# Optimization experiments

Measured on AMD Instinct MI355X. Metric: run time of the kernel, lower is better.

## Reference

```python
import jax, jax.numpy as jnp
import numpy as np

H = 16          # num_heads
HD = 64         # head_dim = latent_dim // num_heads
RHD = 32        # rope_head_dim = head_dim // 2
NHD = 32        # nope_head_dim
Q_LAT = 256     # latent_dim // compression_ratio
KV_LAT = 204    # xf_latent_dim // (compression_ratio + 1)
MAX_LEN = 2048
THETA = 10000.0
EPS = 1e-5


def _rope_tables():
    half = RHD // 2  # 16
    freqs = 1.0 / THETA ** (np.arange(half, dtype=np.float32) / half)
    t = np.arange(MAX_LEN, dtype=np.float32)
    ang = np.outer(t, freqs)  # (MAX_LEN, half)
    return jnp.asarray(np.cos(ang)), jnp.asarray(np.sin(ang))

COS, SIN = _rope_tables()


def _ln(x, g, b):
    m = jnp.mean(x, axis=-1, keepdims=True)
    v = jnp.var(x, axis=-1, keepdims=True)
    return (x - m) * jax.lax.rsqrt(v + EPS) * g + b


def _rope(t, cos, sin):
    # t: (..., L, RHD); cos/sin: (L, RHD//2); interleaved even/odd convention
    ev, od = t[..., 0::2], t[..., 1::2]
    oe = ev * cos - od * sin
    oo = ev * sin + od * cos
    return jnp.stack([oe, oo], axis=-1).reshape(t.shape)


def setup_inputs() -> dict:
    key = jax.random.key(0)
    ks = jax.random.split(key, 12)
    D = 1024
    s = 0.02
    return {
        "x": jax.random.normal(ks[0], (2, 2048, D), jnp.float32),
        "xf": jax.random.normal(ks[1], (2, 2048, D), jnp.float32),
        "Wqc": jax.random.normal(ks[2], (D, Q_LAT), jnp.float32) * s,
        "gq": jnp.ones((Q_LAT,), jnp.float32),
        "bq": jnp.zeros((Q_LAT,), jnp.float32),
        "Wq_rope": jax.random.normal(ks[3], (Q_LAT, H * RHD), jnp.float32) * s,
        "Wq_nope": jax.random.normal(ks[4], (Q_LAT, H * NHD), jnp.float32) * s,
        "Wkvc": jax.random.normal(ks[5], (D, KV_LAT), jnp.float32) * s,
        "gkv": jnp.ones((KV_LAT,), jnp.float32),
        "bkv": jnp.zeros((KV_LAT,), jnp.float32),
        "Wk_nope": jax.random.normal(ks[6], (KV_LAT, H * NHD), jnp.float32) * s,
        "Wv": jax.random.normal(ks[7], (KV_LAT, H * HD), jnp.float32) * s,
        "Wkr": jax.random.normal(ks[8], (D, RHD), jnp.float32) * s,
        "Wo": jax.random.normal(ks[9], (D, D), jnp.float32) * s,
        "bo": jnp.zeros((D,), jnp.float32),
    }


def reference(x, xf, Wqc, gq, bq, Wq_rope, Wq_nope, Wkvc, gkv, bkv, Wk_nope, Wv, Wkr, Wo, bo):
    B, T, D = x.shape
    S = xf.shape[1]

    # query path: compress -> LN -> decoupled decompress
    ql = _ln(x @ Wqc, gq, bq)                                   # (B,T,Q_LAT)
    q_nope = (ql @ Wq_nope).reshape(B, T, H, NHD).transpose(0, 2, 1, 3)  # (B,H,T,NHD)
    q_rope = (ql @ Wq_rope).reshape(B, T, H, RHD).transpose(0, 2, 1, 3)  # (B,H,T,RHD)

    # key/value path: compress -> LN -> decompress; shared single rope head
    kvl = _ln(xf @ Wkvc, gkv, bkv)                              # (B,S,KV_LAT)
    k_nope = (kvl @ Wk_nope).reshape(B, S, H, NHD).transpose(0, 2, 1, 3)  # (B,H,S,NHD)
    v = (kvl @ Wv).reshape(B, S, H, HD).transpose(0, 2, 1, 3)   # (B,H,S,HD)
    k_rope = (xf @ Wkr).reshape(B, S, 1, RHD).transpose(0, 2, 1, 3)       # (B,1,S,RHD)

    q_rope = _rope(q_rope, COS[:T], SIN[:T])
    k_rope = _rope(k_rope, COS[:S], SIN[:S]) / H
    k_rope = jnp.broadcast_to(k_rope, (B, H, S, RHD))

    q = jnp.concatenate([q_nope, q_rope], axis=-1)              # (B,H,T,HD)
    k = jnp.concatenate([k_nope, k_rope], axis=-1)              # (B,H,S,HD)

    scale = 1.0 / jnp.sqrt(jnp.asarray(HD, q.dtype))
    scores = jnp.einsum("bhtd,bhsd->bhts", q, k) * scale
    attn = jax.nn.softmax(scores, axis=-1)
    o = jnp.einsum("bhts,bhsd->bhtd", attn, v)                  # (B,H,T,HD)
    o = o.transpose(0, 2, 1, 3).reshape(B, T, H * HD)
    return o @ Wo + bo
```

## Files before the change

### kernel.cpp

```cpp
#include <hip/hip_runtime.h>
#include <hip/hip_bf16.h>
#include <math.h>

#define SEQ 2048

typedef __bf16 bf16x8 __attribute__((ext_vector_type(8)));
typedef float  f32x4  __attribute__((ext_vector_type(4)));

#if __has_builtin(__builtin_amdgcn_exp2f)
#define EXP2(x) __builtin_amdgcn_exp2f(x)
#else
#define EXP2(x) exp2f(x)
#endif

__device__ __forceinline__ unsigned short f2bf(float f) {
  __bf16 h = (__bf16)f;
  return __builtin_bit_cast(unsigned short, h);
}

__device__ __forceinline__ void gload16(const unsigned short* g, unsigned short* l) {
  __builtin_amdgcn_global_load_lds(
      (const __attribute__((address_space(1))) void*)g,
      (__attribute__((address_space(3))) void*)l, 16, 0, 0);
}

__device__ __forceinline__ unsigned cvtpk(float lo, float hi) {
  unsigned r;
  asm("v_cvt_pk_bf16_f32 %0, %1, %2" : "=v"(r) : "v"(lo), "v"(hi));
  return r;
}
__device__ __forceinline__ void plswap32(unsigned &a, unsigned &b) {
  asm("v_permlane32_swap_b32 %0, %1" : "+v"(a), "+v"(b));
}
__device__ __forceinline__ void plswap16(unsigned &a, unsigned &b) {
  asm("v_permlane16_swap_b32 %0, %1" : "+v"(a), "+v"(b));
}

#define CLOG (0.125f * 1.44269504f)

struct WPrep {
  const float* src[8];
  unsigned short* dst[8];
  int K[8], N[8], NR[8], KC[8], nb[8];
  float2* cst;
};

__global__ __launch_bounds__(256) void wprep_kernel(WPrep p)
{
  __shared__ float tile[32][33];
  int bid = blockIdx.x;
  if (bid < 128) {
    const int idx = bid * 256 + threadIdx.x;
    const int pos = idx >> 4, i = idx & 15;
    const float freq = EXP2(-(float)i * 0.8304820237f);
    const float ang = (float)pos * freq;
    p.cst[idx] = make_float2(cosf(ang), sinf(ang));
    return;
  }
  bid -= 128;
  int di = 0;
  while (bid >= p.nb[di]) { bid -= p.nb[di]; ++di; }
  const float* src = p.src[di];
  unsigned short* dst = p.dst[di];
  const int K = p.K[di], N = p.N[di], KC = p.KC[di];
  const int nkx = KC >> 5;
  const int k0 = (bid % nkx) * 32, n0 = (bid / nkx) * 32;
  const int tx = threadIdx.x & 31, ty = threadIdx.x >> 5;
  for (int r = ty; r < 32; r += 8) {
    const int k = k0 + r, n = n0 + tx;
    tile[r][tx] = (k < K && n < N) ? src[(long)k * N + n] : 0.0f;
  }
  __syncthreads();
  for (int r = ty; r < 32; r += 8) {
    const int n = n0 + r, k = k0 + tx;
    dst[(long)n * KC + k] = f2bf(tile[tx][r]);
  }
}

template <int EPI, bool AF32>
__device__ __forceinline__ void gemm_body(
    unsigned short* smem,
    const void* __restrict__ Av, const unsigned short* __restrict__ BT,
    const float* __restrict__ bias, const float2* __restrict__ cst,
    void* __restrict__ C0v, void* __restrict__ C1v, int K, int N,
    int bx, int by)
{
  unsigned short* As = smem;
  unsigned short* Bs = smem + 2 * 128 * 32;
  const int tid = threadIdx.x;
  const int w = tid >> 6, lane = tid & 63;
  const int ln16 = lane & 15, quad = lane >> 4;
  const int wm = (w >> 1) * 64, wn = (w & 1) * 64;
  const int m0 = by * 128, n0 = bx * 128;
  const int rr = tid >> 2, cc = (tid & 3) * 8;

  const unsigned short* A = (const unsigned short*)Av;

  auto stageB = [&](int ib, int k0) {
    gload16(&BT[(long)(n0 + rr)      * K + k0 + cc], &Bs[ib * 4096 + rr * 32 + cc]);
    gload16(&BT[(long)(n0 + 64 + rr) * K + k0 + cc], &Bs[ib * 4096 + (64 + rr) * 32 + cc]);
  };
  auto stageAbf = [&](int ib, int k0) {
    gload16(&A[(long)(m0 + rr)      * K + k0 + cc], &As[ib * 4096 + rr * 32 + cc]);
    gload16(&A[(long)(m0 + 64 + rr) * K + k0 + cc], &As[ib * 4096 + (64 + rr) * 32 + cc]);
  };

  f32x4 acc[4][4];
#pragma unroll
  for (int i = 0; i < 4; ++i)
#pragma unroll
    for (int j = 0; j < 4; ++j)
#pragma unroll
      for (int r = 0; r < 4; ++r) acc[i][j][r] = 0.0f;

  stageB(0, 0);
  stageAbf(0, 0);

  int ib = 0;
  for (int k0 = 0; k0 < K; k0 += 32, ib ^= 1) {
    __syncthreads();
    const int kn = k0 + 32;
    if (kn < K) { stageB(ib ^ 1, kn); stageAbf(ib ^ 1, kn); }
    bf16x8 fa[4], fb[4];
#pragma unroll
    for (int i = 0; i < 4; ++i) fa[i] = *(const bf16x8*)&As[ib * 4096 + (wm + i * 16 + ln16) * 32 + quad * 8];
#pragma unroll
    for (int j = 0; j < 4; ++j) fb[j] = *(const bf16x8*)&Bs[ib * 4096 + (wn + j * 16 + ln16) * 32 + quad * 8];
#pragma unroll
    for (int i = 0; i < 4; ++i)
#pragma unroll
      for (int j = 0; j < 4; ++j)
        acc[i][j] = __builtin_amdgcn_mfma_f32_16x16x32_bf16(fa[i], fb[j], acc[i][j], 0, 0, 0);
  }

  if (EPI == 5 && n0 >= 512) {
    __syncthreads();
#pragma unroll
    for (int i = 0; i < 4; ++i) {
      const int rl = wm + i * 16 + quad * 4;
#pragma unroll
      for (int j = 0; j < 4; ++j) {
        const int cl = wn + j * 16 + ln16;
        ushort4 u;
        u.x = f2bf(acc[i][j][0]); u.y = f2bf(acc[i][j][1]);
        u.z = f2bf(acc[i][j][2]); u.w = f2bf(acc[i][j][3]);
        *(ushort4*)&smem[cl * 132 + rl] = u;
      }
    }
    __syncthreads();
    unsigned short* vT = (unsigned short*)C1v;
    const int b = m0 >> 11, sbase = m0 & (SEQ - 1);
    for (int q = tid; q < 128 * 16; q += 256) {
      const int cl = q >> 4, sch = (q & 15) * 8;
      bf16x8 val = *(const bf16x8*)&smem[cl * 132 + sch];
      const int c = (n0 - 512) + cl;
      const int hh = c >> 6, dd = c & 63;
      *(bf16x8*)&vT[((long)(b * 16 + hh) * 64 + dd) * SEQ + sbase + sch] = val;
    }
    return;
  }
#pragma unroll
  for (int i = 0; i < 4; ++i) {
    const int row0 = m0 + wm + i * 16 + quad * 4;
#pragma unroll
    for (int j = 0; j < 4; ++j) {
      const int col = n0 + wn + j * 16 + ln16;
      if (EPI == 3) {
        if (n0 < 512) {
          unsigned short* qn = (unsigned short*)C0v;
#pragma unroll
          for (int r = 0; r < 4; ++r) qn[(long)(row0 + r) * 512 + col] = f2bf(acc[i][j][r] * CLOG);
        } else {
          unsigned short* qr = (unsigned short*)C1v;
          const int c = col - 512;
          const int d = c & 31;
#pragma unroll
          for (int r = 0; r < 4; ++r) {
            const float v = acc[i][j][r];
            const float p = __shfl_xor(v, 1);
            const float2 t = cst[((row0 + r) & (SEQ - 1)) * 16 + (d >> 1)];
            const float o = ((d & 1) == 0) ? (v * t.x - p * t.y) : (p * t.y + v * t.x);
            qr[(long)(row0 + r) * 512 + c] = f2bf(o * CLOG);
          }
        }
      } else if (EPI == 5) {
        unsigned short* kn = (unsigned short*)C0v;
#pragma unroll
        for (int r = 0; r < 4; ++r) kn[(long)(row0 + r) * 512 + col] = f2bf(acc[i][j][r]);
      }
    }
  }
}

template <int E0, bool AF0, int E1, bool AF1>
__global__ __launch_bounds__(256) void gemm_dual(
    const void* __restrict__ A0, const unsigned short* __restrict__ BT0,
    void* __restrict__ C00, void* __restrict__ C01, int K0, int N0, int nx0,
    const void* __restrict__ A1, const unsigned short* __restrict__ BT1,
    void* __restrict__ C10, void* __restrict__ C11, int K1, int N1,
    const float2* __restrict__ cst)
{
  __shared__ unsigned short smem[16896];
  if (blockIdx.z == 0) {
    if ((int)blockIdx.x >= nx0) return;
    gemm_body<E0, AF0>(smem, A0, BT0, nullptr, cst, C00, C01, K0, N0, blockIdx.x, blockIdx.y);
  } else {
    gemm_body<E1, AF1>(smem, A1, BT1, nullptr, cst, C10, C11, K1, N1, blockIdx.x, blockIdx.y);
  }
}

template <int EPI, bool AF32>
__device__ __forceinline__ void gemm_body64(
    unsigned short* smem,
    const void* __restrict__ Av, const unsigned short* __restrict__ BT,
    const float* __restrict__ bias, const float2* __restrict__ cst,
    void* __restrict__ C0v, void* __restrict__ C1v, int K, int N,
    int bx, int by)
{
  unsigned short* As = smem;
  unsigned short* Bs = smem + 2 * 64 * 32;
  const int tid = threadIdx.x;
  const int w = tid >> 6, lane = tid & 63;
  const int ln16 = lane & 15, quad = lane >> 4;
  const int wm = (w >> 1) * 32, wn = (w & 1) * 32;
  const int m0 = by * 64, n0 = bx * 64;
  const int rr = tid >> 2, cc = (tid & 3) * 8;

  const unsigned short* A = (const unsigned short*)Av;
  const float* Af = (const float*)Av;

  auto stageB = [&](int ib, int k0) {
    gload16(&BT[(long)(n0 + rr) * K + k0 + cc], &Bs[ib * 2048 + rr * 32 + cc]);
  };
  auto stageAbf = [&](int ib, int k0) {
    gload16(&A[(long)(m0 + rr) * K + k0 + cc], &As[ib * 2048 + rr * 32 + cc]);
  };
  auto writeAf32 = [&](int ib, const float4& a0, const float4& a1) {
    ushort4 u;
    u.x = f2bf(a0.x); u.y = f2bf(a0.y); u.z = f2bf(a0.z); u.w = f2bf(a0.w);
    *(ushort4*)&As[ib * 2048 + rr * 32 + cc] = u;
    u.x = f2bf(a1.x); u.y = f2bf(a1.y); u.z = f2bf(a1.z); u.w = f2bf(a1.w);
    *(ushort4*)&As[ib * 2048 + rr * 32 + cc + 4] = u;
  };

  f32x4 acc[2][2];
#pragma unroll
  for (int i = 0; i < 2; ++i)
#pragma unroll
    for (int j = 0; j < 2; ++j)
#pragma unroll
      for (int r = 0; r < 4; ++r) acc[i][j][r] = 0.0f;

  stageB(0, 0);
  if (AF32) {
    float4 a0 = *(const float4*)&Af[(long)(m0 + rr) * K + cc];
    float4 a1 = *(const float4*)&Af[(long)(m0 + rr) * K + cc + 4];
    writeAf32(0, a0, a1);
  } else {
    stageAbf(0, 0);
  }

  int ib = 0;
  for (int k0 = 0; k0 < K; k0 += 32, ib ^= 1) {
    __syncthreads();
    const int kn = k0 + 32;
    float4 a0, a1;
    if (kn < K) {
      stageB(ib ^ 1, kn);
      if (AF32) {
        a0 = *(const float4*)&Af[(long)(m0 + rr) * K + kn + cc];
        a1 = *(const float4*)&Af[(long)(m0 + rr) * K + kn + cc + 4];
      } else {
        stageAbf(ib ^ 1, kn);
      }
    }
    bf16x8 fa[2], fb[2];
#pragma unroll
    for (int i = 0; i < 2; ++i) fa[i] = *(const bf16x8*)&As[ib * 2048 + (wm + i * 16 + ln16) * 32 + quad * 8];
#pragma unroll
    for (int j = 0; j < 2; ++j) fb[j] = *(const bf16x8*)&Bs[ib * 2048 + (wn + j * 16 + ln16) * 32 + quad * 8];
#pragma unroll
    for (int i = 0; i < 2; ++i)
#pragma unroll
      for (int j = 0; j < 2; ++j)
        acc[i][j] = __builtin_amdgcn_mfma_f32_16x16x32_bf16(fa[i], fb[j], acc[i][j], 0, 0, 0);
    if (AF32 && kn < K) writeAf32(ib ^ 1, a0, a1);
  }

#pragma unroll
  for (int i = 0; i < 2; ++i) {
    const int row0 = m0 + wm + i * 16 + quad * 4;
#pragma unroll
    for (int j = 0; j < 2; ++j) {
      const int col = n0 + wn + j * 16 + ln16;
      if (EPI == 0 || EPI == 1) {
        float* C = (float*)C0v;
        float bv = (EPI == 1) ? bias[col] : 0.0f;
#pragma unroll
        for (int r = 0; r < 4; ++r) C[(long)(row0 + r) * N + col] = acc[i][j][r] + bv;
      } else if (EPI == 4) {
        if (n0 < 256) {
          float* kvl = (float*)C0v;
#pragma unroll
          for (int r = 0; r < 4; ++r) kvl[(long)(row0 + r) * 256 + col] = acc[i][j][r];
        } else if (wn == 0) {
          unsigned short* kr = (unsigned short*)C1v;
          const int d = col - 256;
#pragma unroll
          for (int r = 0; r < 4; ++r) {
            const float v = acc[i][j][r];
            const float p = __shfl_xor(v, 1);
            const float2 t = cst[((row0 + r) & (SEQ - 1)) * 16 + (d >> 1)];
            const float o = ((d & 1) == 0) ? (v * t.x - p * t.y) : (p * t.y + v * t.x);
            kr[(long)(row0 + r) * 32 + d] = f2bf(o * 0.0625f);
          }
        }
      }
    }
  }
}

template <int EPI, bool AF32>
__global__ __launch_bounds__(256) void gemm_mfma64(
    const void* __restrict__ Av, const unsigned short* __restrict__ BT,
    const float* __restrict__ bias, const float2* __restrict__ cst,
    void* __restrict__ C0v, void* __restrict__ C1v, int K, int N)
{
  __shared__ unsigned short smem[8192];
  gemm_body64<EPI, AF32>(smem, Av, BT, bias, cst, C0v, C1v, K, N, blockIdx.x, blockIdx.y);
}

template <int E0, bool AF0, int E1, bool AF1>
__global__ __launch_bounds__(256) void gemm_dual64(
    const void* __restrict__ A0, const unsigned short* __restrict__ BT0,
    void* __restrict__ C00, void* __restrict__ C01, int K0, int N0, int nx0,
    const void* __restrict__ A1, const unsigned short* __restrict__ BT1,
    void* __restrict__ C10, void* __restrict__ C11, int K1, int N1,
    const float2* __restrict__ cst)
{
  __shared__ unsigned short smem[8192];
  if (blockIdx.z == 0) {
    if ((int)blockIdx.x >= nx0) return;
    gemm_body64<E0, AF0>(smem, A0, BT0, nullptr, cst, C00, C01, K0, N0, blockIdx.x, blockIdx.y);
  } else {
    gemm_body64<E1, AF1>(smem, A1, BT1, nullptr, cst, C10, C11, K1, N1, blockIdx.x, blockIdx.y);
  }
}

__global__ __launch_bounds__(256) void ln2_kernel(
    const float* __restrict__ Xq, const float* __restrict__ Xkv,
    const float* __restrict__ gq, const float* __restrict__ bq,
    const float* __restrict__ gkv, const float* __restrict__ bkv,
    unsigned short* __restrict__ Yq, unsigned short* __restrict__ Ykv)
{
  const int row0 = blockIdx.x, tid = threadIdx.x;
  const bool isq = row0 < 4096;
  const int row = isq ? row0 : row0 - 4096;
  const float* X = isq ? Xq : Xkv;
  const float* g = isq ? gq : gkv;
  const float* b = isq ? bq : bkv;
  unsigned short* Y = isq ? Yq : Ykv;
  const int C = isq ? 256 : 204;
  const int Cp = isq ? 256 : 224;
  float v = (tid < C) ? X[(long)row * 256 + tid] : 0.0f;
  float s1 = v, s2 = v * v;
#pragma unroll
  for (int off = 1; off < 64; off <<= 1) {
    s1 += __shfl_xor(s1, off);
    s2 += __shfl_xor(s2, off);
  }
  __shared__ float rA[4], rB[4];
  const int wid = tid >> 6;
  if ((tid & 63) == 0) { rA[wid] = s1; rB[wid] = s2; }
  __syncthreads();
  s1 = rA[0] + rA[1] + rA[2] + rA[3];
  s2 = rB[0] + rB[1] + rB[2] + rB[3];
  const float mean = s1 / C;
  const float var  = s2 / C - mean * mean;
  const float r = rsqrtf(var + 1e-5f);
  if (tid < C) Y[(long)row * Cp + tid] = f2bf((v - mean) * r * g[tid] + b[tid]);
  else if (tid < Cp) Y[(long)row * Cp + tid] = 0;
}

#define KSTR 36
#define VSTR 68
__global__ __launch_bounds__(256, 2) void attn_mfma_kernel(
    const unsigned short* __restrict__ qn, const unsigned short* __restrict__ qr,
    const unsigned short* __restrict__ kn, const unsigned short* __restrict__ kr,
    const unsigned short* __restrict__ vT, unsigned short* __restrict__ ob)
{
  __shared__ unsigned short Kn[2][64 * KSTR];
  __shared__ unsigned short Vs[2][64 * VSTR];
  const int id = blockIdx.x;
  const int xcd = id & 7, j = id >> 3;
  const int bh = xcd * 4 + (j & 3);
  const int tile = j >> 2;
  const int b = bh >> 4, h = bh & 15;
  const int t0 = tile * 128;
  const int tid = threadIdx.x;
  const int w = tid >> 6, lane = tid & 63;
  const int ln16 = lane & 15, quad = lane >> 4;
  const int trow = w * 16;
  const long bT = (long)b * SEQ;

  const int krow = tid >> 2, kc8 = (tid & 3) * 8;
  const int vd0 = tid >> 3, vc0 = (tid & 7) * 8;
  const int vd1 = vd0 + 32;

  bf16x8 q0A = *(const bf16x8*)&qn[(bT + t0 + trow + ln16) * 512 + h * 32 + quad * 8];
  bf16x8 q1A = *(const bf16x8*)&qr[(bT + t0 + trow + ln16) * 512 + h * 32 + quad * 8];
  bf16x8 q0B = *(const bf16x8*)&qn[(bT + t0 + 64 + trow + ln16) * 512 + h * 32 + quad * 8];
  bf16x8 q1B = *(const bf16x8*)&qr[(bT + t0 + 64 + trow + ln16) * 512 + h * 32 + quad * 8];

  auto loadKV = [&](int s0, bf16x8& rk0, bf16x8& rv0, bf16x8& rv1) {
    rk0 = *(const bf16x8*)&kn[(bT + s0 + krow) * 512 + h * 32 + kc8];
    rv0 = *(const bf16x8*)&vT[((long)bh * 64 + vd0) * SEQ + s0 + vc0];
    rv1 = *(const bf16x8*)&vT[((long)bh * 64 + vd1) * SEQ + s0 + vc0];
  };
  auto writeKV = [&](int ib, bf16x8 rk0, bf16x8 rv0, bf16x8 rv1) {
    *(bf16x8*)&Kn[ib][krow * KSTR + kc8] = rk0;
    *(bf16x8*)&Vs[ib][vd0 * VSTR + vc0] = rv0;
    *(bf16x8*)&Vs[ib][vd1 * VSTR + vc0] = rv1;
  };
  auto loadKrF = [&](int s0, bf16x8* f) {
#pragma unroll
    for (int nt = 0; nt < 4; ++nt)
      f[nt] = *(const bf16x8*)&kr[(bT + s0 + nt * 16 + ln16) * 32 + quad * 8];
  };
  auto pxform = [&](const f32x4* sf, float& l_part, bf16x8& a0, bf16x8& a1) {
    float p[16];
#pragma unroll
    for (int nt = 0; nt < 4; ++nt)
#pragma unroll
      for (int r = 0; r < 4; ++r) {
        const float e = EXP2(sf[nt][r]);
        p[nt * 4 + r] = e;
        l_part += e;
      }
    unsigned u0 = cvtpk(p[0],  p[1]),  u1 = cvtpk(p[2],  p[3]);
    unsigned u2 = cvtpk(p[4],  p[5]),  u3 = cvtpk(p[6],  p[7]);
    unsigned u4 = cvtpk(p[8],  p[9]),  u5 = cvtpk(p[10], p[11]);
    unsigned u6 = cvtpk(p[12], p[13]), u7 = cvtpk(p[14], p[15]);
    plswap32(u0, u2); plswap16(u0, u2);
    plswap32(u1, u3); plswap16(u1, u3);
    plswap32(u4, u6); plswap16(u4, u6);
    plswap32(u5, u7); plswap16(u5, u7);
    const uint4 w0 = make_uint4(u0, u1, u2, u3);
    const uint4 w1 = make_uint4(u4, u5, u6, u7);
    a0 = __builtin_bit_cast(bf16x8, w0);
    a1 = __builtin_bit_cast(bf16x8, w1);
  };

  bf16x8 ck0, cv0, cv1;
  bf16x8 nk0, nv0, nv1;
  bf16x8 ckr[4];
  loadKV(0, ck0, cv0, cv1);
  writeKV(0, ck0, cv0, cv1);
  loadKV(64, nk0, nv0, nv1);
  loadKrF(0, ckr);

  f32x4 o_acc[2][4];
#pragma unroll
  for (int g = 0; g < 2; ++g)
#pragma unroll
    for (int nt = 0; nt < 4; ++nt)
#pragma unroll
      for (int r = 0; r < 4; ++r) o_acc[g][nt][r] = 0.0f;
  float l_part[2] = {0.0f, 0.0f};

  int ib = 0;
  for (int s0 = 0; s0 < SEQ; s0 += 64, ib ^= 1) {
    __syncthreads();
    if (s0 + 64 < SEQ) {
      writeKV(ib ^ 1, nk0, nv0, nv1);
      if (s0 + 128 < SEQ) loadKV(s0 + 128, nk0, nv0, nv1);
    }

    bf16x8 ka[4];
#pragma unroll
    for (int nt = 0; nt < 4; ++nt)
      ka[nt] = *(const bf16x8*)&Kn[ib][(nt * 16 + ln16) * KSTR + quad * 8];

    f32x4 sfA[4], sfB[4];
#pragma unroll
    for (int nt = 0; nt < 4; ++nt)
#pragma unroll
      for (int r = 0; r < 4; ++r) { sfA[nt][r] = 0.0f; sfB[nt][r] = 0.0f; }
#pragma unroll
    for (int nt = 0; nt < 4; ++nt) {
      sfA[nt] = __builtin_amdgcn_mfma_f32_16x16x32_bf16(ka[nt], q0A, sfA[nt], 0, 0, 0);
      sfA[nt] = __builtin_amdgcn_mfma_f32_16x16x32_bf16(ckr[nt], q1A, sfA[nt], 0, 0, 0);
    }
#pragma unroll
    for (int nt = 0; nt < 4; ++nt) {
      sfB[nt] = __builtin_amdgcn_mfma_f32_16x16x32_bf16(ka[nt], q0B, sfB[nt], 0, 0, 0);
      sfB[nt] = __builtin_amdgcn_mfma_f32_16x16x32_bf16(ckr[nt], q1B, sfB[nt], 0, 0, 0);
    }

    if (s0 + 64 < SEQ) loadKrF(s0 + 64, ckr);

    bf16x8 a0A, a1A, a0B, a1B;
    pxform(sfA, l_part[0], a0A, a1A);
    pxform(sfB, l_part[1], a0B, a1B);

#pragma unroll
    for (int nt = 0; nt < 4; ++nt) {
      bf16x8 v0 = *(const bf16x8*)&Vs[ib][(nt * 16 + ln16) * VSTR + quad * 8];
      o_acc[0][nt] = __builtin_amdgcn_mfma_f32_16x16x32_bf16(a0A, v0, o_acc[0][nt], 0, 0, 0);
      o_acc[1][nt] = __builtin_amdgcn_mfma_f32_16x16x32_bf16(a0B, v0, o_acc[1][nt], 0, 0, 0);
      bf16x8 v1 = *(const bf16x8*)&Vs[ib][(nt * 16 + ln16) * VSTR + 32 + quad * 8];
      o_acc[0][nt] = __builtin_amdgcn_mfma_f32_16x16x32_bf16(a1A, v1, o_acc[0][nt], 0, 0, 0);
      o_acc[1][nt] = __builtin_amdgcn_mfma_f32_16x16x32_bf16(a1B, v1, o_acc[1][nt], 0, 0, 0);
    }
  }

#pragma unroll
  for (int g = 0; g < 2; ++g) {
    float l_i = l_part[g];
    l_i += __shfl_xor(l_i, 16);
    l_i += __shfl_xor(l_i, 32);
    const float lr = 1.0f / l_i;
    float lq[4];
#pragma unroll
    for (int r = 0; r < 4; ++r) lq[r] = __shfl(lr, quad * 4 + r);
#pragma unroll
    for (int r = 0; r < 4; ++r) {
      const long t = t0 + g * 64 + trow + quad * 4 + r;
      const long base = (bT + t) * 1024 + h * 64 + ln16;
#pragma unroll
      for (int nt = 0; nt < 4; ++nt)
        ob[base + nt * 16] = f2bf(o_acc[g][nt][r] * lq[r]);
    }
  }
}

extern "C" void kernel_launch(void* const* d_in, const int* in_sizes, int n_in,
                              void* d_out, int out_size, void* d_ws, size_t ws_size,
                              hipStream_t stream) {
  const float* x       = (const float*)d_in[0];
  const float* xf      = (const float*)d_in[1];
  const float* Wqc     = (const float*)d_in[2];
  const float* gq      = (const float*)d_in[3];
  const float* bq      = (const float*)d_in[4];
  const float* Wq_rope = (const float*)d_in[5];
  const float* Wq_nope = (const float*)d_in[6];
  const float* Wkvc    = (const float*)d_in[7];
  const float* gkv     = (const float*)d_in[8];
  const float* bkv     = (const float*)d_in[9];
  const float* Wk_nope = (const float*)d_in[10];
  const float* Wv      = (const float*)d_in[11];
  const float* Wkr     = (const float*)d_in[12];
  const float* Wo      = (const float*)d_in[13];
  const float* bo      = (const float*)d_in[14];
  float* out = (float*)d_out;

  const long R = 4096;
  float* ws = (float*)d_ws;
  float* ql_f  = ws;
  float* kvl_f = ql_f + R * 256;
  float2* cst  = (float2*)(kvl_f + R * 256);
  unsigned short* us = (unsigned short*)(cst + 2048 * 16);
  unsigned short* ql_bf  = us;  us += R * 256;
  unsigned short* kvl_bf = us;  us += R * 224;
  unsigned short* qn_bf  = us;  us += R * 512;
  unsigned short* qr_bf  = us;  us += R * 512;
  unsigned short* kn_bf  = us;  us += R * 512;
  unsigned short* kr_bf  = us;  us += R * 32;
  unsigned short* vT_bf  = us;  us += R * 1024;
  unsigned short* o_bf   = us;  us += R * 1024;
  unsigned short* WqcT   = us;  us += 256 * 1024;
  unsigned short* WkvkrT = us;  us += 384 * 1024;
  unsigned short* WqnqrT = us;  us += 1024 * 256;
  unsigned short* WknvT  = us;  us += 1536 * 224;
  unsigned short* WoT    = us;  us += 1024 * 1024;

  WPrep p;
  const float* srcs[8] = {Wqc, Wkvc, Wkr, Wq_nope, Wq_rope, Wk_nope, Wv, Wo};
  unsigned short* dsts[8] = {WqcT, WkvkrT, WkvkrT + 256 * 1024,
                             WqnqrT, WqnqrT + 512 * 256,
                             WknvT, WknvT + 512 * 224, WoT};
  const int Ks[8]  = {1024, 1024, 1024, 256, 256, 204, 204, 1024};
  const int Ns[8]  = {256, 204, 32, 512, 512, 512, 1024, 1024};
  const int NRs[8] = {256, 256, 128, 512, 512, 512, 1024, 1024};
  const int KCs[8] = {1024, 1024, 1024, 256, 256, 224, 224, 1024};
  int total = 128;
  for (int i = 0; i < 8; ++i) {
    p.src[i] = srcs[i]; p.dst[i] = dsts[i];
    p.K[i] = Ks[i]; p.N[i] = Ns[i]; p.NR[i] = NRs[i]; p.KC[i] = KCs[i];
    p.nb[i] = (KCs[i] / 32) * (NRs[i] / 32);
    total += p.nb[i];
  }
  p.cst = cst;
  wprep_kernel<<<total, 256, 0, stream>>>(p);

  gemm_dual64<0, true, 4, true><<<dim3(6, 64, 2), 256, 0, stream>>>(
      x, WqcT, ql_f, nullptr, 1024, 256, 4,
      xf, WkvkrT, kvl_f, kr_bf, 1024, 384, cst);
  ln2_kernel<<<8192, 256, 0, stream>>>(ql_f, kvl_f, gq, bq, gkv, bkv, ql_bf, kvl_bf);
  gemm_dual<3, false, 5, false><<<dim3(12, 32, 2), 256, 0, stream>>>(
      ql_bf, WqnqrT, qn_bf, qr_bf, 256, 1024, 8,
      kvl_bf, WknvT, kn_bf, vT_bf, 224, 1536, cst);
  attn_mfma_kernel<<<512, 256, 0, stream>>>(qn_bf, qr_bf, kn_bf, kr_bf, vT_bf, o_bf);
  gemm_mfma64<1, false><<<dim3(16, 64), 256, 0, stream>>>(o_bf, WoT, bo, nullptr, out, nullptr, 1024, 1024);
}
```

Before: 224.0 us.

## Load K/V fragments directly from global into registers, dropping LDS staging

```diff
diff --git a/kernel.cpp b/kernel.cpp
--- a/kernel.cpp
+++ b/kernel.cpp
@@ -382,15 +382,11 @@
   else if (tid < Cp) Y[(long)row * Cp + tid] = 0;
 }
 
-#define KSTR 36
-#define VSTR 68
 __global__ __launch_bounds__(256, 2) void attn_mfma_kernel(
     const unsigned short* __restrict__ qn, const unsigned short* __restrict__ qr,
     const unsigned short* __restrict__ kn, const unsigned short* __restrict__ kr,
     const unsigned short* __restrict__ vT, unsigned short* __restrict__ ob)
 {
-  __shared__ unsigned short Kn[2][64 * KSTR];
-  __shared__ unsigned short Vs[2][64 * VSTR];
   const int id = blockIdx.x;
   const int xcd = id & 7, j = id >> 3;
   const int bh = xcd * 4 + (j & 3);
@@ -403,31 +399,30 @@
   const int trow = w * 16;
   const long bT = (long)b * SEQ;
 
-  const int krow = tid >> 2, kc8 = (tid & 3) * 8;
-  const int vd0 = tid >> 3, vc0 = (tid & 7) * 8;
-  const int vd1 = vd0 + 32;
-
   bf16x8 q0A = *(const bf16x8*)&qn[(bT + t0 + trow + ln16) * 512 + h * 32 + quad * 8];
   bf16x8 q1A = *(const bf16x8*)&qr[(bT + t0 + trow + ln16) * 512 + h * 32 + quad * 8];
   bf16x8 q0B = *(const bf16x8*)&qn[(bT + t0 + 64 + trow + ln16) * 512 + h * 32 + quad * 8];
   bf16x8 q1B = *(const bf16x8*)&qr[(bT + t0 + 64 + trow + ln16) * 512 + h * 32 + quad * 8];
 
-  auto loadKV = [&](int s0, bf16x8& rk0, bf16x8& rv0, bf16x8& rv1) {
-    rk0 = *(const bf16x8*)&kn[(bT + s0 + krow) * 512 + h * 32 + kc8];
-    rv0 = *(const bf16x8*)&vT[((long)bh * 64 + vd0) * SEQ + s0 + vc0];
-    rv1 = *(const bf16x8*)&vT[((long)bh * 64 + vd1) * SEQ + s0 + vc0];
-  };
-  auto writeKV = [&](int ib, bf16x8 rk0, bf16x8 rv0, bf16x8 rv1) {
-    *(bf16x8*)&Kn[ib][krow * KSTR + kc8] = rk0;
-    *(bf16x8*)&Vs[ib][vd0 * VSTR + vc0] = rv0;
-    *(bf16x8*)&Vs[ib][vd1 * VSTR + vc0] = rv1;
-  };
-  auto loadKrF = [&](int s0, bf16x8* f) {
-#pragma unroll
-    for (int nt = 0; nt < 4; ++nt)
-      f[nt] = *(const bf16x8*)&kr[(bT + s0 + nt * 16 + ln16) * 32 + quad * 8];
-  };
-  auto pxform = [&](const f32x4* sf, float& l_part, bf16x8& a0, bf16x8& a1) {
+  const unsigned short* kbase  = &kn[(bT + ln16) * 512 + h * 32 + quad * 8];
+  const unsigned short* krbase = &kr[(bT + ln16) * 32 + quad * 8];
+  const unsigned short* vbase  = &vT[((long)bh * 64 + ln16) * SEQ + quad * 8];
+
+  auto loadK = [&](int s0, bf16x8* k, bf16x8* krf) {
+#pragma unroll
+    for (int nt = 0; nt < 4; ++nt) {
+      k[nt]   = *(const bf16x8*)&kbase [(long)(s0 + nt * 16) * 512];
+      krf[nt] = *(const bf16x8*)&krbase[(long)(s0 + nt * 16) * 32];
+    }
+  };
+  auto loadV = [&](int s0, bf16x8* v0, bf16x8* v1) {
+#pragma unroll
+    for (int nt = 0; nt < 4; ++nt) {
+      v0[nt] = *(const bf16x8*)&vbase[(long)nt * 16 * SEQ + s0];
+      v1[nt] = *(const bf16x8*)&vbase[(long)nt * 16 * SEQ + s0 + 32];
+    }
+  };
+  auto pxform = [&](const f32x4* sf, float& l_acc, bf16x8& a0, bf16x8& a1) {
     float p[16];
 #pragma unroll
     for (int nt = 0; nt < 4; ++nt)
@@ -435,7 +430,7 @@
       for (int r = 0; r < 4; ++r) {
         const float e = EXP2(sf[nt][r]);
         p[nt * 4 + r] = e;
-        l_part += e;
+        l_acc += e;
       }
     unsigned u0 = cvtpk(p[0],  p[1]),  u1 = cvtpk(p[2],  p[3]);
     unsigned u2 = cvtpk(p[4],  p[5]),  u3 = cvtpk(p[6],  p[7]);
@@ -451,14 +446,6 @@
     a1 = __builtin_bit_cast(bf16x8, w1);
   };
 
-  bf16x8 ck0, cv0, cv1;
-  bf16x8 nk0, nv0, nv1;
-  bf16x8 ckr[4];
-  loadKV(0, ck0, cv0, cv1);
-  writeKV(0, ck0, cv0, cv1);
-  loadKV(64, nk0, nv0, nv1);
-  loadKrF(0, ckr);
-
   f32x4 o_acc[2][4];
 #pragma unroll
   for (int g = 0; g < 2; ++g)
@@ -468,36 +455,21 @@
       for (int r = 0; r < 4; ++r) o_acc[g][nt][r] = 0.0f;
   float l_part[2] = {0.0f, 0.0f};
 
-  int ib = 0;
-  for (int s0 = 0; s0 < SEQ; s0 += 64, ib ^= 1) {
-    __syncthreads();
-    if (s0 + 64 < SEQ) {
-      writeKV(ib ^ 1, nk0, nv0, nv1);
-      if (s0 + 128 < SEQ) loadKV(s0 + 128, nk0, nv0, nv1);
-    }
-
-    bf16x8 ka[4];
+  auto step = [&](int s0, bf16x8* k, bf16x8* krf, bf16x8* v0, bf16x8* v1) {
+    f32x4 sfA[4], sfB[4];
 #pragma unroll
     for (int nt = 0; nt < 4; ++nt)
-      ka[nt] = *(const bf16x8*)&Kn[ib][(nt * 16 + ln16) * KSTR + quad * 8];
-
-    f32x4 sfA[4], sfB[4];
-#pragma unroll
-    for (int nt = 0; nt < 4; ++nt)
 #pragma unroll
       for (int r = 0; r < 4; ++r) { sfA[nt][r] = 0.0f; sfB[nt][r] = 0.0f; }
 #pragma unroll
     for (int nt = 0; nt < 4; ++nt) {
-      sfA[nt] = __builtin_amdgcn_mfma_f32_16x16x32_bf16(ka[nt], q0A, sfA[nt], 0, 0, 0);
-      sfA[nt] = __builtin_amdgcn_mfma_f32_16x16x32_bf16(ckr[nt], q1A, sfA[nt], 0, 0, 0);
-    }
-#pragma unroll
-    for (int nt = 0; nt < 4; ++nt) {
-      sfB[nt] = __builtin_amdgcn_mfma_f32_16x16x32_bf16(ka[nt], q0B, sfB[nt], 0, 0, 0);
-      sfB[nt] = __builtin_amdgcn_mfma_f32_16x16x32_bf16(ckr[nt], q1B, sfB[nt], 0, 0, 0);
-    }
-
-    if (s0 + 64 < SEQ) loadKrF(s0 + 64, ckr);
+      sfA[nt] = __builtin_amdgcn_mfma_f32_16x16x32_bf16(k[nt],   q0A, sfA[nt], 0, 0, 0);
+      sfA[nt] = __builtin_amdgcn_mfma_f32_16x16x32_bf16(krf[nt], q1A, sfA[nt], 0, 0, 0);
+      sfB[nt] = __builtin_amdgcn_mfma_f32_16x16x32_bf16(k[nt],   q0B, sfB[nt], 0, 0, 0);
+      sfB[nt] = __builtin_amdgcn_mfma_f32_16x16x32_bf16(krf[nt], q1B, sfB[nt], 0, 0, 0);
+    }
+    const int sp = s0 + 128;
+    if (sp < SEQ) loadK(sp, k, krf);
 
     bf16x8 a0A, a1A, a0B, a1B;
     pxform(sfA, l_part[0], a0A, a1A);
@@ -505,13 +477,22 @@
 
 #pragma unroll
     for (int nt = 0; nt < 4; ++nt) {
-      bf16x8 v0 = *(const bf16x8*)&Vs[ib][(nt * 16 + ln16) * VSTR + quad * 8];
-      o_acc[0][nt] = __builtin_amdgcn_mfma_f32_16x16x32_bf16(a0A, v0, o_acc[0][nt], 0, 0, 0);
-      o_acc[1][nt] = __builtin_amdgcn_mfma_f32_16x16x32_bf16(a0B, v0, o_acc[1][nt], 0, 0, 0);
-      bf16x8 v1 = *(const bf16x8*)&Vs[ib][(nt * 16 + ln16) * VSTR + 32 + quad * 8];
-      o_acc[0][nt] = __builtin_amdgcn_mfma_f32_16x16x32_bf16(a1A, v1, o_acc[0][nt], 0, 0, 0);
-      o_acc[1][nt] = __builtin_amdgcn_mfma_f32_16x16x32_bf16(a1B, v1, o_acc[1][nt], 0, 0, 0);
-    }
+      o_acc[0][nt] = __builtin_amdgcn_mfma_f32_16x16x32_bf16(a0A, v0[nt], o_acc[0][nt], 0, 0, 0);
+      o_acc[1][nt] = __builtin_amdgcn_mfma_f32_16x16x32_bf16(a0B, v0[nt], o_acc[1][nt], 0, 0, 0);
+      o_acc[0][nt] = __builtin_amdgcn_mfma_f32_16x16x32_bf16(a1A, v1[nt], o_acc[0][nt], 0, 0, 0);
+      o_acc[1][nt] = __builtin_amdgcn_mfma_f32_16x16x32_bf16(a1B, v1[nt], o_acc[1][nt], 0, 0, 0);
+    }
+    if (sp < SEQ) loadV(sp, v0, v1);
+  };
+
+  bf16x8 kA[4], krA[4], vA0[4], vA1[4];
+  bf16x8 kB[4], krB[4], vB0[4], vB1[4];
+  loadK(0, kA, krA);   loadV(0, vA0, vA1);
+  loadK(64, kB, krB);  loadV(64, vB0, vB1);
+
+  for (int s0 = 0; s0 < SEQ; s0 += 128) {
+    step(s0,      kA, krA, vA0, vA1);
+    step(s0 + 64, kB, krB, vB0, vB1);
   }
 
 #pragma unroll
```

New measurement: 280.8 us. +25.4%, slower.

## Pre-convert x/xf to bf16 in prep kernel and widen GEMM tiles to 64x128

Applied to the files above, without the earlier changes.

```diff
diff --git a/kernel.cpp b/kernel.cpp
--- a/kernel.cpp
+++ b/kernel.cpp
@@ -43,6 +43,8 @@
   unsigned short* dst[8];
   int K[8], N[8], NR[8], KC[8], nb[8];
   float2* cst;
+  const float* xs[2];
+  unsigned short* xd[2];
 };
 
 __global__ __launch_bounds__(256) void wprep_kernel(WPrep p)
@@ -58,6 +60,19 @@
     return;
   }
   bid -= 128;
+  if (bid < 4096) {
+    const int sel = bid >> 11;
+    const long base = (long)(bid & 2047) * 2048 + threadIdx.x * 8;
+    const float4 a = *(const float4*)&p.xs[sel][base];
+    const float4 b = *(const float4*)&p.xs[sel][base + 4];
+    ushort4 u0, u1;
+    u0.x = f2bf(a.x); u0.y = f2bf(a.y); u0.z = f2bf(a.z); u0.w = f2bf(a.w);
+    u1.x = f2bf(b.x); u1.y = f2bf(b.y); u1.z = f2bf(b.z); u1.w = f2bf(b.w);
+    *(ushort4*)&p.xd[sel][base] = u0;
+    *(ushort4*)&p.xd[sel][base + 4] = u1;
+    return;
+  }
+  bid -= 4096;
   int di = 0;
   while (bid >= p.nb[di]) { bid -= p.nb[di]; ++di; }
   const float* src = p.src[di];
@@ -209,101 +224,76 @@
   }
 }
 
-template <int EPI, bool AF32>
-__device__ __forceinline__ void gemm_body64(
+template <int EPI>
+__device__ __forceinline__ void gemm_wbody(
     unsigned short* smem,
-    const void* __restrict__ Av, const unsigned short* __restrict__ BT,
+    const unsigned short* __restrict__ A, const unsigned short* __restrict__ BT,
     const float* __restrict__ bias, const float2* __restrict__ cst,
     void* __restrict__ C0v, void* __restrict__ C1v, int K, int N,
     int bx, int by)
 {
   unsigned short* As = smem;
-  unsigned short* Bs = smem + 2 * 64 * 32;
+  unsigned short* Bs = smem + 4096;
   const int tid = threadIdx.x;
   const int w = tid >> 6, lane = tid & 63;
   const int ln16 = lane & 15, quad = lane >> 4;
-  const int wm = (w >> 1) * 32, wn = (w & 1) * 32;
-  const int m0 = by * 64, n0 = bx * 64;
+  const int wm = (w >> 1) * 32, wn = (w & 1) * 64;
+  const int m0 = by * 64, n0 = bx * 128;
   const int rr = tid >> 2, cc = (tid & 3) * 8;
 
-  const unsigned short* A = (const unsigned short*)Av;
-  const float* Af = (const float*)Av;
-
+  auto stageA = [&](int ib, int k0) {
+    gload16(&A[(long)(m0 + rr) * K + k0 + cc], &As[ib * 2048 + rr * 32 + cc]);
+  };
   auto stageB = [&](int ib, int k0) {
-    gload16(&BT[(long)(n0 + rr) * K + k0 + cc], &Bs[ib * 2048 + rr * 32 + cc]);
-  };
-  auto stageAbf = [&](int ib, int k0) {
-    gload16(&A[(long)(m0 + rr) * K + k0 + cc], &As[ib * 2048 + rr * 32 + cc]);
-  };
-  auto writeAf32 = [&](int ib, const float4& a0, const float4& a1) {
-    ushort4 u;
-    u.x = f2bf(a0.x); u.y = f2bf(a0.y); u.z = f2bf(a0.z); u.w = f2bf(a0.w);
-    *(ushort4*)&As[ib * 2048 + rr * 32 + cc] = u;
-    u.x = f2bf(a1.x); u.y = f2bf(a1.y); u.z = f2bf(a1.z); u.w = f2bf(a1.w);
-    *(ushort4*)&As[ib * 2048 + rr * 32 + cc + 4] = u;
-  };
-
-  f32x4 acc[2][2];
+    gload16(&BT[(long)(n0 + rr)      * K + k0 + cc], &Bs[ib * 4096 + rr * 32 + cc]);
+    gload16(&BT[(long)(n0 + 64 + rr) * K + k0 + cc], &Bs[ib * 4096 + (64 + rr) * 32 + cc]);
+  };
+
+  f32x4 acc[2][4];
 #pragma unroll
   for (int i = 0; i < 2; ++i)
 #pragma unroll
-    for (int j = 0; j < 2; ++j)
+    for (int j = 0; j < 4; ++j)
 #pragma unroll
       for (int r = 0; r < 4; ++r) acc[i][j][r] = 0.0f;
 
+  stageA(0, 0);
   stageB(0, 0);
-  if (AF32) {
-    float4 a0 = *(const float4*)&Af[(long)(m0 + rr) * K + cc];
-    float4 a1 = *(const float4*)&Af[(long)(m0 + rr) * K + cc + 4];
-    writeAf32(0, a0, a1);
-  } else {
-    stageAbf(0, 0);
-  }
 
   int ib = 0;
   for (int k0 = 0; k0 < K; k0 += 32, ib ^= 1) {
     __syncthreads();
     const int kn = k0 + 32;
-    float4 a0, a1;
-    if (kn < K) {
-      stageB(ib ^ 1, kn);
-      if (AF32) {
-        a0 = *(const float4*)&Af[(long)(m0 + rr) * K + kn + cc];
-        a1 = *(const float4*)&Af[(long)(m0 + rr) * K + kn + cc + 4];
-      } else {
-        stageAbf(ib ^ 1, kn);
-      }
-    }
-    bf16x8 fa[2], fb[2];
+    if (kn < K) { stageA(ib ^ 1, kn); stageB(ib ^ 1, kn); }
+    bf16x8 fa[2], fb[4];
 #pragma unroll
     for (int i = 0; i < 2; ++i) fa[i] = *(const bf16x8*)&As[ib * 2048 + (wm + i * 16 + ln16) * 32 + quad * 8];
 #pragma unroll
-    for (int j = 0; j < 2; ++j) fb[j] = *(const bf16x8*)&Bs[ib * 2048 + (wn + j * 16 + ln16) * 32 + quad * 8];
+    for (int j = 0; j < 4; ++j) fb[j] = *(const bf16x8*)&Bs[ib * 4096 + (wn + j * 16 + ln16) * 32 + quad * 8];
 #pragma unroll
     for (int i = 0; i < 2; ++i)
 #pragma unroll
-      for (int j = 0; j < 2; ++j)
+      for (int j = 0; j < 4; ++j)
         acc[i][j] = __builtin_amdgcn_mfma_f32_16x16x32_bf16(fa[i], fb[j], acc[i][j], 0, 0, 0);
-    if (AF32 && kn < K) writeAf32(ib ^ 1, a0, a1);
   }
 
 #pragma unroll
   for (int i = 0; i < 2; ++i) {
     const int row0 = m0 + wm + i * 16 + quad * 4;
 #pragma unroll
-    for (int j = 0; j < 2; ++j) {
+    for (int j = 0; j < 4; ++j) {
       const int col = n0 + wn + j * 16 + ln16;
       if (EPI == 0 || EPI == 1) {
         float* C = (float*)C0v;
-        float bv = (EPI == 1) ? bias[col] : 0.0f;
+        const float bv = (EPI == 1) ? bias[col] : 0.0f;
 #pragma unroll
         for (int r = 0; r < 4; ++r) C[(long)(row0 + r) * N + col] = acc[i][j][r] + bv;
       } else if (EPI == 4) {
-        if (n0 < 256) {
+        if (col < 256) {
           float* kvl = (float*)C0v;
 #pragma unroll
           for (int r = 0; r < 4; ++r) kvl[(long)(row0 + r) * 256 + col] = acc[i][j][r];
-        } else if (wn == 0) {
+        } else if (col < 288) {
           unsigned short* kr = (unsigned short*)C1v;
           const int d = col - 256;
 #pragma unroll
@@ -320,30 +310,30 @@
   }
 }
 
-template <int EPI, bool AF32>
-__global__ __launch_bounds__(256) void gemm_mfma64(
-    const void* __restrict__ Av, const unsigned short* __restrict__ BT,
+template <int EPI>
+__global__ __launch_bounds__(256) void gemm_widek(
+    const unsigned short* __restrict__ A, const unsigned short* __restrict__ BT,
     const float* __restrict__ bias, const float2* __restrict__ cst,
-    void* __restrict__ C0v, void* __restrict__ C1v, int K, int N)
-{
-  __shared__ unsigned short smem[8192];
-  gemm_body64<EPI, AF32>(smem, Av, BT, bias, cst, C0v, C1v, K, N, blockIdx.x, blockIdx.y);
-}
-
-template <int E0, bool AF0, int E1, bool AF1>
-__global__ __launch_bounds__(256) void gemm_dual64(
-    const void* __restrict__ A0, const unsigned short* __restrict__ BT0,
+    void* __restrict__ C0, void* __restrict__ C1, int K, int N)
+{
+  __shared__ unsigned short smem[12288];
+  gemm_wbody<EPI>(smem, A, BT, bias, cst, C0, C1, K, N, blockIdx.x, blockIdx.y);
+}
+
+template <int E0, int E1>
+__global__ __launch_bounds__(256) void gemm_dualw(
+    const unsigned short* __restrict__ A0, const unsigned short* __restrict__ BT0,
     void* __restrict__ C00, void* __restrict__ C01, int K0, int N0, int nx0,
-    const void* __restrict__ A1, const unsigned short* __restrict__ BT1,
+    const unsigned short* __restrict__ A1, const unsigned short* __restrict__ BT1,
     void* __restrict__ C10, void* __restrict__ C11, int K1, int N1,
     const float2* __restrict__ cst)
 {
-  __shared__ unsigned short smem[8192];
+  __shared__ unsigned short smem[12288];
   if (blockIdx.z == 0) {
     if ((int)blockIdx.x >= nx0) return;
-    gemm_body64<E0, AF0>(smem, A0, BT0, nullptr, cst, C00, C01, K0, N0, blockIdx.x, blockIdx.y);
+    gemm_wbody<E0>(smem, A0, BT0, nullptr, cst, C00, C01, K0, N0, blockIdx.x, blockIdx.y);
   } else {
-    gemm_body64<E1, AF1>(smem, A1, BT1, nullptr, cst, C10, C11, K1, N1, blockIdx.x, blockIdx.y);
+    gemm_wbody<E1>(smem, A1, BT1, nullptr, cst, C10, C11, K1, N1, blockIdx.x, blockIdx.y);
   }
 }
 
@@ -568,6 +558,8 @@
   unsigned short* kr_bf  = us;  us += R * 32;
   unsigned short* vT_bf  = us;  us += R * 1024;
   unsigned short* o_bf   = us;  us += R * 1024;
+  unsigned short* x_bf   = us;  us += R * 1024;
+  unsigned short* xf_bf  = us;  us += R * 1024;
   unsigned short* WqcT   = us;  us += 256 * 1024;
   unsigned short* WkvkrT = us;  us += 384 * 1024;
   unsigned short* WqnqrT = us;  us += 1024 * 256;
@@ -583,7 +575,7 @@
   const int Ns[8]  = {256, 204, 32, 512, 512, 512, 1024, 1024};
   const int NRs[8] = {256, 256, 128, 512, 512, 512, 1024, 1024};
   const int KCs[8] = {1024, 1024, 1024, 256, 256, 224, 224, 1024};
-  int total = 128;
+  int total = 128 + 4096;
   for (int i = 0; i < 8; ++i) {
     p.src[i] = srcs[i]; p.dst[i] = dsts[i];
     p.K[i] = Ks[i]; p.N[i] = Ns[i]; p.NR[i] = NRs[i]; p.KC[i] = KCs[i];
@@ -591,15 +583,17 @@
     total += p.nb[i];
   }
   p.cst = cst;
+  p.xs[0] = x;  p.xs[1] = xf;
+  p.xd[0] = x_bf; p.xd[1] = xf_bf;
   wprep_kernel<<<total, 256, 0, stream>>>(p);
 
-  gemm_dual64<0, true, 4, true><<<dim3(6, 64, 2), 256, 0, stream>>>(
-      x, WqcT, ql_f, nullptr, 1024, 256, 4,
-      xf, WkvkrT, kvl_f, kr_bf, 1024, 384, cst);
+  gemm_dualw<0, 4><<<dim3(3, 64, 2), 256, 0, stream>>>(
+      x_bf, WqcT, ql_f, nullptr, 1024, 256, 2,
+      xf_bf, WkvkrT, kvl_f, kr_bf, 1024, 384, cst);
   ln2_kernel<<<8192, 256, 0, stream>>>(ql_f, kvl_f, gq, bq, gkv, bkv, ql_bf, kvl_bf);
   gemm_dual<3, false, 5, false><<<dim3(12, 32, 2), 256, 0, stream>>>(
       ql_bf, WqnqrT, qn_bf, qr_bf, 256, 1024, 8,
       kvl_bf, WknvT, kn_bf, vT_bf, 224, 1536, cst);
   attn_mfma_kernel<<<512, 256, 0, stream>>>(qn_bf, qr_bf, kn_bf, kr_bf, vT_bf, o_bf);
-  gemm_mfma64<1, false><<<dim3(16, 64), 256, 0, stream>>>(o_bf, WoT, bo, nullptr, out, nullptr, 1024, 1024);
-}
+  gemm_widek<1><<<dim3(8, 64), 256, 0, stream>>>(o_bf, WoT, bo, cst, out, nullptr, 1024, 1024);
+}
```

After: 211.5 us. 1.06x faster.
